# Kernel tuning notes

Measured on AMD Instinct MI355X. Metric: run time of the kernel, lower is better.

The kernel has to match this reference:

```python
import jax, jax.numpy as jnp
import numpy as np

N, E, IN, HID, OUT, H, R = 50000, 800000, 128, 64, 64, 4, 64
NEG_SLOPE = 0.2


def setup_inputs() -> dict:
    key = jax.random.key(0)
    ks = jax.random.split(key, 20)
    s = 0.05
    inp = {
        "x": jax.random.normal(ks[0], (N, IN), jnp.float32),
        "edge_index": jax.random.randint(ks[1], (2, E), 0, N, jnp.int32),
        "edge_type": jax.random.randint(ks[2], (E,), 0, R, jnp.int32),
        # layer 1 (in -> hidden)
        "rel1": jax.random.normal(ks[3], (R, IN), jnp.float32) * s,
        "W1": jax.random.normal(ks[4], (IN, H * HID), jnp.float32) * s,
        "We1": jax.random.normal(ks[5], (IN, H * HID), jnp.float32) * s,
        "as1": jax.random.normal(ks[6], (H, HID), jnp.float32) * s,
        "ad1": jax.random.normal(ks[7], (H, HID), jnp.float32) * s,
        "ae1": jax.random.normal(ks[8], (H, HID), jnp.float32) * s,
        "b1": jnp.zeros((HID,), jnp.float32),
        # layer 2 (hidden -> out)
        "rel2": jax.random.normal(ks[9], (R, HID), jnp.float32) * s,
        "W2": jax.random.normal(ks[10], (HID, H * OUT), jnp.float32) * s,
        "We2": jax.random.normal(ks[11], (HID, H * OUT), jnp.float32) * s,
        "as2": jax.random.normal(ks[12], (H, OUT), jnp.float32) * s,
        "ad2": jax.random.normal(ks[13], (H, OUT), jnp.float32) * s,
        "ae2": jax.random.normal(ks[14], (H, OUT), jnp.float32) * s,
        "b2": jnp.zeros((OUT,), jnp.float32),
    }
    return inp


def gat_layer(x, src, dst, edge_type, rel, W, We, a_s, a_d, a_e, b, C):
    # x: [N, Din] -> per-head features [N, H, C]
    xs = (x @ W).reshape(-1, H, C)
    alpha_src = jnp.einsum('nhc,hc->nh', xs, a_s)   # [N,H]
    alpha_dst = jnp.einsum('nhc,hc->nh', xs, a_d)   # [N,H]
    e = (rel[edge_type] @ We).reshape(-1, H, C)     # [E,H,C] projected edge feats
    alpha_e = jnp.einsum('ehc,hc->eh', e, a_e)      # [E,H]
    logits = alpha_src[src] + alpha_dst[dst] + alpha_e
    logits = jnp.where(logits >= 0, logits, NEG_SLOPE * logits)  # leaky_relu
    # segment softmax over destination nodes
    lmax = jax.ops.segment_max(logits, dst, num_segments=N)      # [N,H]
    ex = jnp.exp(logits - lmax[dst])
    den = jax.ops.segment_sum(ex, dst, num_segments=N)           # [N,H]
    w = ex / den[dst]                                            # [E,H]
    msg = w[:, :, None] * xs[src]                                # [E,H,C]
    out = jax.ops.segment_sum(msg, dst, num_segments=N)          # [N,H,C]
    return out.mean(axis=1) + b                                  # concat=False -> head mean


def reference(x, edge_index, edge_type, rel1, W1, We1, as1, ad1, ae1, b1,
              rel2, W2, We2, as2, ad2, ae2, b2):
    src, dst = edge_index[0], edge_index[1]
    h = gat_layer(x, src, dst, edge_type, rel1, W1, We1, as1, ad1, ae1, b1, HID)
    h = jax.nn.relu(h)
    out = gat_layer(h, src, dst, edge_type, rel2, W2, We2, as2, ad2, ae2, b2, OUT)
    return out
```

## Files before the change

kernel.cpp:

```cpp
#include <hip/hip_runtime.h>
#include <hip/hip_bf16.h>
#include <hip/hip_fp16.h>
#include <math.h>

#define N_NODES 50000
#define N_EDGES 800000
#define IN_DIM 128
#define NHEAD 4
#define NREL 64
#define HC 256
#define NEG_SLOPE 0.2f
#define SCAN_B ((N_NODES + 255) / 256)

using short8 = __attribute__((ext_vector_type(8))) short;
using f32x4  = __attribute__((ext_vector_type(4))) float;

__device__ __forceinline__ void load_lds16s(const short* g, short* l) {
  __builtin_amdgcn_global_load_lds(
      (const __attribute__((address_space(1))) unsigned int*)g,
      (__attribute__((address_space(3))) unsigned int*)l, 16, 0, 0);
}

__device__ __forceinline__ unsigned bf16rne(float v) {
  unsigned u = __float_as_uint(v);
  return (u + 0x7FFFu + ((u >> 16) & 1u)) >> 16;
}

__global__ __launch_bounds__(256) void prep_x(
    const float* __restrict__ X, short* __restrict__ Xh, short* __restrict__ Xl,
    int K) {
  __shared__ float plds[16 * 132];
  const int t = threadIdx.x;
  const int blk = blockIdx.x;
  const int LW = K + 4;
  for (int i = t * 4; i < 16 * K; i += 1024) {
    int r = i / K, k = i - r * K;
    *(float4*)&plds[r * LW + k] = *(const float4*)&X[(size_t)(blk * 16 + r) * K + k];
  }
  __syncthreads();
  for (int c = t; c < 2 * K; c += 256) {
    int p_k = c >> 6, l = c & 63;
    int r = l & 15, k0 = p_k * 32 + (l >> 4) * 8;
    unsigned hp[4], lp[4];
#pragma unroll
    for (int q = 0; q < 4; ++q) {
      float v0 = plds[r * LW + k0 + q * 2];
      float v1 = plds[r * LW + k0 + q * 2 + 1];
      unsigned h0 = bf16rne(v0), h1 = bf16rne(v1);
      float l0 = (v0 - __uint_as_float(h0 << 16)) * 256.0f;
      float l1 = (v1 - __uint_as_float(h1 << 16)) * 256.0f;
      hp[q] = h0 | (h1 << 16);
      lp[q] = bf16rne(l0) | (bf16rne(l1) << 16);
    }
    size_t base = ((size_t)(blk * (K >> 5) + p_k) * 64 + l) * 8;
    *(int4*)&Xh[base] = make_int4(hp[0], hp[1], hp[2], hp[3]);
    *(int4*)&Xl[base] = make_int4(lp[0], lp[1], lp[2], lp[3]);
  }
}

__global__ __launch_bounds__(256) void prep_w(
    const float* __restrict__ W, short* __restrict__ Wh, short* __restrict__ Wl,
    int K) {
  const int c = blockIdx.x * 256 + threadIdx.x;
  const int KP = K >> 5;
  if (c >= 16 * KP * 64) return;
  const int p = c >> 6, l = c & 63;
  const int p_c = p / KP, p_k = p - p_c * KP;
  const int col = p_c * 16 + (l & 15), k0 = p_k * 32 + (l >> 4) * 8;
  unsigned hp[4], lp[4];
#pragma unroll
  for (int q = 0; q < 4; ++q) {
    float v0 = W[(size_t)(k0 + q * 2) * HC + col];
    float v1 = W[(size_t)(k0 + q * 2 + 1) * HC + col];
    unsigned h0 = bf16rne(v0), h1 = bf16rne(v1);
    float l0 = (v0 - __uint_as_float(h0 << 16)) * 256.0f;
    float l1 = (v1 - __uint_as_float(h1 << 16)) * 256.0f;
    hp[q] = h0 | (h1 << 16);
    lp[q] = bf16rne(l0) | (bf16rne(l1) << 16);
  }
  size_t base = (size_t)c * 8;
  *(int4*)&Wh[base] = make_int4(hp[0], hp[1], hp[2], hp[3]);
  *(int4*)&Wl[base] = make_int4(lp[0], lp[1], lp[2], lp[3]);
}

__global__ __launch_bounds__(256, 4) void gemm_mfma(
    const short* __restrict__ Xh, const short* __restrict__ Xl,
    const short* __restrict__ Wh, const short* __restrict__ Wl,
    const float* __restrict__ a_s, const float* __restrict__ a_d,
    __half2* __restrict__ xs16, float* __restrict__ asrc, float* __restrict__ adst,
    int M, int K) {
  __shared__ short lds[2][24 * 512];
  const int t = threadIdx.x;
  const int wv = t >> 6, l = t & 63;
  const int KP = K >> 5;
  const int pr0 = blockIdx.x * 4;
  const int pc0 = blockIdx.y * 8;
  const int c0 = blockIdx.y * 128;

#define STAGE(BI, PK)                                                         \
  {                                                                           \
    _Pragma("unroll")                                                         \
    for (int j = 0; j < 6; ++j) {                                             \
      const int s = wv * 6 + j;                                               \
      const short* srcp;                                                      \
      if (s < 4)       srcp = Xh + (((size_t)(pr0 + s) * KP + (PK)) << 9);    \
      else if (s < 8)  srcp = Xl + (((size_t)(pr0 + s - 4) * KP + (PK)) << 9);\
      else if (s < 16) srcp = Wh + (((size_t)(pc0 + s - 8) * KP + (PK)) << 9);\
      else             srcp = Wl + (((size_t)(pc0 + s - 16) * KP + (PK)) << 9);\
      load_lds16s(srcp + l * 8, &lds[BI][s * 512]);                           \
    }                                                                         \
  }

  f32x4 acc0[8], acc1[8];
#pragma unroll
  for (int i = 0; i < 8; ++i)
#pragma unroll
    for (int c = 0; c < 4; ++c) { acc0[i][c] = 0.f; acc1[i][c] = 0.f; }

  STAGE(0, 0);
  for (int pk = 0; pk < KP; ++pk) {
    const int cur = pk & 1;
    if (pk + 1 < KP) {
      STAGE(cur ^ 1, pk + 1);
      asm volatile("s_waitcnt vmcnt(6)" ::: "memory");
    } else {
      asm volatile("s_waitcnt vmcnt(0)" ::: "memory");
    }
    __builtin_amdgcn_s_barrier();
    __builtin_amdgcn_sched_barrier(0);
    const short8 ah = *(const short8*)&lds[cur][(0 + wv) * 512 + l * 8];
    const short8 al = *(const short8*)&lds[cur][(4 + wv) * 512 + l * 8];
#pragma unroll
    for (int t8 = 0; t8 < 8; ++t8) {
      const short8 bh = *(const short8*)&lds[cur][(8 + t8) * 512 + l * 8];
      const short8 bl = *(const short8*)&lds[cur][(16 + t8) * 512 + l * 8];
      acc0[t8] = __builtin_amdgcn_mfma_f32_16x16x32_bf16(ah, bh, acc0[t8], 0, 0, 0);
      acc1[t8] = __builtin_amdgcn_mfma_f32_16x16x32_bf16(ah, bl, acc1[t8], 0, 0, 0);
      acc1[t8] = __builtin_amdgcn_mfma_f32_16x16x32_bf16(al, bh, acc1[t8], 0, 0, 0);
    }
    asm volatile("" ::: "memory");
    __builtin_amdgcn_s_barrier();
  }
#undef STAGE

  const int col_l = l & 15;
  const int row_l = (l >> 4) * 2 * 2;
  __half* xsh = (__half*)xs16;
  float asv[8], adv[8];
#pragma unroll
  for (int t8 = 0; t8 < 8; ++t8) {
    asv[t8] = a_s[c0 + t8 * 16 + col_l];
    adv[t8] = a_d[c0 + t8 * 16 + col_l];
  }
  float sp[2][4], dp[2][4];
#pragma unroll
  for (int hl = 0; hl < 2; ++hl)
#pragma unroll
    for (int r = 0; r < 4; ++r) { sp[hl][r] = 0.f; dp[hl][r] = 0.f; }

#pragma unroll
  for (int t8 = 0; t8 < 8; ++t8) {
    const int hl = t8 >> 2;
#pragma unroll
    for (int r = 0; r < 4; ++r) {
      const float v = acc0[t8][r] + acc1[t8][r] * (1.0f / 256.0f);
      const int row = (pr0 + wv) * 16 + row_l + r;
      if (row < M) {
        const int col = c0 + t8 * 16 + col_l;
        xsh[(size_t)row * HC + col] = __float2half(v);
      }
      sp[hl][r] += v * asv[t8];
      dp[hl][r] += v * adv[t8];
    }
  }
#pragma unroll
  for (int off = 1; off < 16; off <<= 1) {
#pragma unroll
    for (int hl = 0; hl < 2; ++hl)
#pragma unroll
      for (int r = 0; r < 4; ++r) {
        sp[hl][r] += __shfl_xor(sp[hl][r], off);
        dp[hl][r] += __shfl_xor(dp[hl][r], off);
      }
  }
  if (col_l == 0) {
#pragma unroll
    for (int hl = 0; hl < 2; ++hl) {
      const int head = blockIdx.y * 2 + hl;
#pragma unroll
      for (int r = 0; r < 4; ++r) {
        const int row = (pr0 + wv) * 16 + row_l + r;
        if (row < M) {
          asrc[row * NHEAD + head] = sp[hl][r];
          adst[row * NHEAD + head] = dp[hl][r];
        }
      }
    }
  }
}

__global__ __launch_bounds__(256) void relalpha2_kernel(
    const float* __restrict__ rel1, const float* __restrict__ We1, const float* __restrict__ ae1,
    const float* __restrict__ rel2, const float* __restrict__ We2, const float* __restrict__ ae2,
    float* __restrict__ tab1, float* __restrict__ tab2) {
  const int layer = blockIdx.x >> 6;
  const int r = blockIdx.x & 63;
  const float* rel = layer ? rel2 : rel1;
  const float* We  = layer ? We2  : We1;
  const float* ae  = layer ? ae2  : ae1;
  float* tab       = layer ? tab2 : tab1;
  const int K      = layer ? 64   : IN_DIM;
  int t = threadIdx.x;
  float acc = 0.f;
  for (int k = 0; k < K; ++k) acc += rel[(size_t)r * K + k] * We[(size_t)k * HC + t];
  int h = t >> 6, lane = t & 63;
  float p = acc * ae[t];
#pragma unroll
  for (int off = 32; off > 0; off >>= 1) p += __shfl_down(p, off);
  if (lane == 0) tab[r * NHEAD + h] = p;
}

__global__ __launch_bounds__(256) void hist_kernel(
    const int* __restrict__ dst, int* __restrict__ deg) {
  int e = blockIdx.x * blockDim.x + threadIdx.x;
  if (e < N_EDGES) atomicAdd(&deg[dst[e]], 1);
}

__global__ __launch_bounds__(256) void block_sum_kernel(
    const int* __restrict__ deg, int* __restrict__ bsum) {
  int i = blockIdx.x * 256 + threadIdx.x;
  int v = (i < N_NODES) ? deg[i] : 0;
#pragma unroll
  for (int off = 32; off > 0; off >>= 1) v += __shfl_down(v, off);
  __shared__ int w[4];
  if ((threadIdx.x & 63) == 0) w[threadIdx.x >> 6] = v;
  __syncthreads();
  if (threadIdx.x == 0) bsum[blockIdx.x] = w[0] + w[1] + w[2] + w[3];
}

__global__ __launch_bounds__(256) void scan_bsum_kernel(
    const int* __restrict__ bsum, int* __restrict__ boff) {
  __shared__ int s[256];
  int t = threadIdx.x;
  int v = (t < SCAN_B) ? bsum[t] : 0;
  s[t] = v;
  __syncthreads();
  for (int off = 1; off < 256; off <<= 1) {
    int u = (t >= off) ? s[t - off] : 0;
    __syncthreads();
    s[t] += u;
    __syncthreads();
  }
  boff[t] = (t == 0) ? 0 : s[t - 1];
}

__global__ __launch_bounds__(256) void scan_final_kernel(
    const int* __restrict__ deg, const int* __restrict__ boff,
    int* __restrict__ rowptr, int* __restrict__ cursor) {
  __shared__ int s[256];
  int t = threadIdx.x;
  int i = blockIdx.x * 256 + t;
  int v = (i < N_NODES) ? deg[i] : 0;
  s[t] = v;
  __syncthreads();
  for (int off = 1; off < 256; off <<= 1) {
    int u = (t >= off) ? s[t - off] : 0;
    __syncthreads();
    s[t] += u;
    __syncthreads();
  }
  int excl = boff[blockIdx.x] + s[t] - v;
  if (i < N_NODES) {
    rowptr[i] = excl;
    cursor[i] = excl;
  }
  if (t == 0 && blockIdx.x == 0) rowptr[N_NODES] = N_EDGES;
}

__global__ __launch_bounds__(256) void fill_kernel(
    const int* __restrict__ src, const int* __restrict__ dst,
    const int* __restrict__ etype, int* __restrict__ cursor,
    int2* __restrict__ csr_pack) {
  int e = blockIdx.x * blockDim.x + threadIdx.x;
  if (e >= N_EDGES) return;
  int d = dst[e];
  int i = atomicAdd(&cursor[d], 1);
  csr_pack[i] = make_int2(src[e], etype[e]);
}

__global__ __launch_bounds__(256) void gat_node_kernel(
    const int* __restrict__ rowptr, const int2* __restrict__ csr,
    const float* __restrict__ asrc, const float* __restrict__ adst,
    const float* __restrict__ tab, const __half2* __restrict__ xs16,
    const float* __restrict__ b, float* __restrict__ out, int relu) {
  const int n = (blockIdx.x * blockDim.x + threadIdx.x) >> 6;
  if (n >= N_NODES) return;
  const int lane = threadIdx.x & 63;
  const int hh = lane >> 4;
  const int cbase = lane << 2;
  const int i0 = rowptr[n], i1 = rowptr[n + 1];
  const float adn = adst[n * NHEAD + hh];
  const float treg = tab[lane * NHEAD + hh];

  float4 acc = make_float4(0.f, 0.f, 0.f, 0.f);
  float den = 0.f;
  int i = i0;
  for (; i + 4 <= i1; i += 4) {
    const int2 p0 = csr[i], p1 = csr[i + 1], p2 = csr[i + 2], p3 = csr[i + 3];
    float l0 = asrc[p0.x * NHEAD + hh] + adn + __shfl(treg, p0.y);
    float l1 = asrc[p1.x * NHEAD + hh] + adn + __shfl(treg, p1.y);
    float l2 = asrc[p2.x * NHEAD + hh] + adn + __shfl(treg, p2.y);
    float l3 = asrc[p3.x * NHEAD + hh] + adn + __shfl(treg, p3.y);
    const uint2 q0 = *(const uint2*)&xs16[((size_t)p0.x * HC + cbase) >> 1];
    const uint2 q1 = *(const uint2*)&xs16[((size_t)p1.x * HC + cbase) >> 1];
    const uint2 q2 = *(const uint2*)&xs16[((size_t)p2.x * HC + cbase) >> 1];
    const uint2 q3 = *(const uint2*)&xs16[((size_t)p3.x * HC + cbase) >> 1];
    l0 = (l0 >= 0.f) ? l0 : NEG_SLOPE * l0;
    l1 = (l1 >= 0.f) ? l1 : NEG_SLOPE * l1;
    l2 = (l2 >= 0.f) ? l2 : NEG_SLOPE * l2;
    l3 = (l3 >= 0.f) ? l3 : NEG_SLOPE * l3;
    const float w0 = __expf(l0), w1 = __expf(l1), w2 = __expf(l2), w3 = __expf(l3);
    den += (w0 + w1) + (w2 + w3);
    const float2 a0 = __half22float2(*(const __half2*)&q0.x), b0 = __half22float2(*(const __half2*)&q0.y);
    const float2 a1 = __half22float2(*(const __half2*)&q1.x), b1 = __half22float2(*(const __half2*)&q1.y);
    const float2 a2 = __half22float2(*(const __half2*)&q2.x), b2 = __half22float2(*(const __half2*)&q2.y);
    const float2 a3 = __half22float2(*(const __half2*)&q3.x), b3 = __half22float2(*(const __half2*)&q3.y);
    acc.x += w0 * a0.x + w1 * a1.x + w2 * a2.x + w3 * a3.x;
    acc.y += w0 * a0.y + w1 * a1.y + w2 * a2.y + w3 * a3.y;
    acc.z += w0 * b0.x + w1 * b1.x + w2 * b2.x + w3 * b3.x;
    acc.w += w0 * b0.y + w1 * b1.y + w2 * b2.y + w3 * b3.y;
  }
  for (; i < i1; ++i) {
    const int2 p = csr[i];
    float l = asrc[p.x * NHEAD + hh] + adn + __shfl(treg, p.y);
    l = (l >= 0.f) ? l : NEG_SLOPE * l;
    const float w = __expf(l);
    const uint2 q = *(const uint2*)&xs16[((size_t)p.x * HC + cbase) >> 1];
    const float2 a = __half22float2(*(const __half2*)&q.x);
    const float2 c = __half22float2(*(const __half2*)&q.y);
    den += w;
    acc.x += w * a.x; acc.y += w * a.y; acc.z += w * c.x; acc.w += w * c.y;
  }

  const float rd = (den > 0.f) ? (0.25f / den) : 0.f;
  float4 y = make_float4(acc.x * rd, acc.y * rd, acc.z * rd, acc.w * rd);
#pragma unroll
  for (int off = 16; off < 64; off <<= 1) {
    y.x += __shfl_xor(y.x, off);
    y.y += __shfl_xor(y.y, off);
    y.z += __shfl_xor(y.z, off);
    y.w += __shfl_xor(y.w, off);
  }
  if (lane < 16) {
    const float4 bb = *(const float4*)&b[lane * 4];
    y.x += bb.x; y.y += bb.y; y.z += bb.z; y.w += bb.w;
    if (relu) {
      y.x = fmaxf(y.x, 0.f); y.y = fmaxf(y.y, 0.f);
      y.z = fmaxf(y.z, 0.f); y.w = fmaxf(y.w, 0.f);
    }
    *(float4*)&out[(size_t)n * 64 + lane * 4] = y;
  }
}

extern "C" void kernel_launch(void* const* d_in, const int* in_sizes, int n_in,
                              void* d_out, int out_size, void* d_ws, size_t ws_size,
                              hipStream_t stream) {
  const float* x   = (const float*)d_in[0];
  const int* eidx  = (const int*)d_in[1];
  const int* etype = (const int*)d_in[2];
  const float* rel1 = (const float*)d_in[3];
  const float* W1   = (const float*)d_in[4];
  const float* We1  = (const float*)d_in[5];
  const float* as1  = (const float*)d_in[6];
  const float* ad1  = (const float*)d_in[7];
  const float* ae1  = (const float*)d_in[8];
  const float* b1   = (const float*)d_in[9];
  const float* rel2 = (const float*)d_in[10];
  const float* W2   = (const float*)d_in[11];
  const float* We2  = (const float*)d_in[12];
  const float* as2  = (const float*)d_in[13];
  const float* ad2  = (const float*)d_in[14];
  const float* ae2  = (const float*)d_in[15];
  const float* b2   = (const float*)d_in[16];
  const int* src = eidx;
  const int* dst = eidx + N_EDGES;

  char* wsb = (char*)d_ws;
  size_t off = 0;
  auto carve = [&](size_t bytes) { char* p = wsb + off; off = (off + bytes + 255) & ~(size_t)255; return p; };
  __half2* xs16 = (__half2*)carve((size_t)N_NODES * HC * 2);
  float* asrc = (float*)carve((size_t)N_NODES * NHEAD * 4);
  float* adst = (float*)carve((size_t)N_NODES * NHEAD * 4);
  float* tab1 = (float*)carve(NREL * NHEAD * 4);
  float* tab2 = (float*)carve(NREL * NHEAD * 4);
  float* h1   = (float*)carve((size_t)N_NODES * 64 * 4);
  short* xfh  = (short*)carve(((size_t)N_NODES * IN_DIM + 32768) * 2);
  short* xfl  = (short*)carve(((size_t)N_NODES * IN_DIM + 32768) * 2);
  short* w1h  = (short*)carve(256 * IN_DIM * 2);
  short* w1l  = (short*)carve(256 * IN_DIM * 2);
  short* w2h  = (short*)carve(256 * 64 * 2);
  short* w2l  = (short*)carve(256 * 64 * 2);
  int* deg    = (int*)carve(N_NODES * 4);
  int* rowptr = (int*)carve((N_NODES + 1) * 4);
  int* cursor = (int*)carve(N_NODES * 4);
  int2* csr   = (int2*)carve((size_t)N_EDGES * 8);
  int* bsum   = (int*)carve(256 * 4);
  int* boff   = (int*)carve(256 * 4);

  hipMemsetAsync(deg, 0, N_NODES * sizeof(int), stream);
  hist_kernel<<<(N_EDGES + 255) / 256, 256, 0, stream>>>(dst, deg);
  block_sum_kernel<<<SCAN_B, 256, 0, stream>>>(deg, bsum);
  scan_bsum_kernel<<<1, 256, 0, stream>>>(bsum, boff);
  scan_final_kernel<<<SCAN_B, 256, 0, stream>>>(deg, boff, rowptr, cursor);
  fill_kernel<<<(N_EDGES + 255) / 256, 256, 0, stream>>>(src, dst, etype, cursor, csr);
  relalpha2_kernel<<<2 * NREL, 256, 0, stream>>>(rel1, We1, ae1, rel2, We2, ae2, tab1, tab2);
  prep_w<<<(16 * (IN_DIM >> 5) * 64 + 255) / 256, 256, 0, stream>>>(W1, w1h, w1l, IN_DIM);
  prep_w<<<(16 * (64 >> 5) * 64 + 255) / 256, 256, 0, stream>>>(W2, w2h, w2l, 64);

  const dim3 gemm_grid((N_NODES + 63) / 64, 2);
  const int GB = (N_NODES * 64 + 255) / 256;
  const int XB = N_NODES / 16;

  prep_x<<<XB, 256, 0, stream>>>(x, xfh, xfl, IN_DIM);
  gemm_mfma<<<gemm_grid, 256, 0, stream>>>(xfh, xfl, w1h, w1l, as1, ad1, xs16, asrc, adst, N_NODES, IN_DIM);
  gat_node_kernel<<<GB, 256, 0, stream>>>(rowptr, csr, asrc, adst, tab1, xs16, b1, h1, 1);

  prep_x<<<XB, 256, 0, stream>>>(h1, xfh, xfl, 64);
  gemm_mfma<<<gemm_grid, 256, 0, stream>>>(xfh, xfl, w2h, w2l, as2, ad2, xs16, asrc, adst, N_NODES, 64);
  gat_node_kernel<<<GB, 256, 0, stream>>>(rowptr, csr, asrc, adst, tab2, xs16, b2, (float*)d_out, 0);
}
```

Baseline: 318.6 us.

## Fuse prep kernels, merge CSR fill into GEMM, emit bf16 split from layer-1

Several small setup kernels (x split, degree histogram, relation alpha table, W splits) are merged into one launch with block-range dispatch. The CSR fill runs as extra blocks in the first GEMM launch, and layer-1 aggregation writes the hi/lo bf16 tiled layout directly, so the h1 buffer and the second prep_x pass go away. This cuts launch count and a full read/write of the hidden activations. In exchange, heterogeneous blocks share one launch, and the fill's atomics now run alongside MFMA work.

New measurement: 309.5 us. 2.9% less time.

```diff
diff --git a/kernel.cpp b/kernel.cpp
--- a/kernel.cpp
+++ b/kernel.cpp
@@ -11,6 +11,9 @@
 #define HC 256
 #define NEG_SLOPE 0.2f
 #define SCAN_B ((N_NODES + 255) / 256)
+#define XB (N_NODES / 16)
+#define HB ((N_EDGES + 255) / 256)
+#define GEMM_BLKS (((N_NODES + 63) / 64) * 2)
 
 using short8 = __attribute__((ext_vector_type(8))) short;
 using f32x4  = __attribute__((ext_vector_type(4))) float;
@@ -26,76 +29,120 @@
   return (u + 0x7FFFu + ((u >> 16) & 1u)) >> 16;
 }
 
-__global__ __launch_bounds__(256) void prep_x(
-    const float* __restrict__ X, short* __restrict__ Xh, short* __restrict__ Xl,
-    int K) {
+__global__ __launch_bounds__(256) void fused_prep(
+    const float* __restrict__ x, short* __restrict__ xfh, short* __restrict__ xfl,
+    const int* __restrict__ dst, int* __restrict__ deg,
+    const float* __restrict__ rel1, const float* __restrict__ We1, const float* __restrict__ ae1,
+    const float* __restrict__ rel2, const float* __restrict__ We2, const float* __restrict__ ae2,
+    float* __restrict__ tab1, float* __restrict__ tab2,
+    const float* __restrict__ W1, short* __restrict__ w1h, short* __restrict__ w1l,
+    const float* __restrict__ W2, short* __restrict__ w2h, short* __restrict__ w2l) {
+  const int bid = blockIdx.x;
+  const int t = threadIdx.x;
   __shared__ float plds[16 * 132];
-  const int t = threadIdx.x;
-  const int blk = blockIdx.x;
-  const int LW = K + 4;
-  for (int i = t * 4; i < 16 * K; i += 1024) {
-    int r = i / K, k = i - r * K;
-    *(float4*)&plds[r * LW + k] = *(const float4*)&X[(size_t)(blk * 16 + r) * K + k];
-  }
-  __syncthreads();
-  for (int c = t; c < 2 * K; c += 256) {
-    int p_k = c >> 6, l = c & 63;
-    int r = l & 15, k0 = p_k * 32 + (l >> 4) * 8;
+
+  if (bid < XB) {
+    const int K = IN_DIM, LW = K + 4;
+    for (int i = t * 4; i < 16 * K; i += 1024) {
+      int r = i / K, k = i - r * K;
+      *(float4*)&plds[r * LW + k] = *(const float4*)&x[(size_t)(bid * 16 + r) * K + k];
+    }
+    __syncthreads();
+    for (int c = t; c < 2 * K; c += 256) {
+      int p_k = c >> 6, l = c & 63;
+      int r = l & 15, k0 = p_k * 32 + (l >> 4) * 8;
+      unsigned hp[4], lp[4];
+#pragma unroll
+      for (int q = 0; q < 4; ++q) {
+        float v0 = plds[r * LW + k0 + q * 2];
+        float v1 = plds[r * LW + k0 + q * 2 + 1];
+        unsigned h0 = bf16rne(v0), h1 = bf16rne(v1);
+        float l0 = (v0 - __uint_as_float(h0 << 16)) * 256.0f;
+        float l1 = (v1 - __uint_as_float(h1 << 16)) * 256.0f;
+        hp[q] = h0 | (h1 << 16);
+        lp[q] = bf16rne(l0) | (bf16rne(l1) << 16);
+      }
+      size_t base = ((size_t)(bid * (K >> 5) + p_k) * 64 + l) * 8;
+      *(int4*)&xfh[base] = make_int4(hp[0], hp[1], hp[2], hp[3]);
+      *(int4*)&xfl[base] = make_int4(lp[0], lp[1], lp[2], lp[3]);
+    }
+    return;
+  }
+  if (bid < XB + HB) {
+    const int e = (bid - XB) * 256 + t;
+    if (e < N_EDGES) atomicAdd(&deg[dst[e]], 1);
+    return;
+  }
+  if (bid < XB + HB + 128) {
+    const int rb = bid - (XB + HB);
+    const int layer = rb >> 6, r = rb & 63;
+    const float* rel = layer ? rel2 : rel1;
+    const float* We  = layer ? We2  : We1;
+    const float* ae  = layer ? ae2  : ae1;
+    float* tab       = layer ? tab2 : tab1;
+    const int K      = layer ? 64   : IN_DIM;
+    float acc = 0.f;
+    for (int k = 0; k < K; ++k) acc += rel[(size_t)r * K + k] * We[(size_t)k * HC + t];
+    int h = t >> 6, lane = t & 63;
+    float p = acc * ae[t];
+#pragma unroll
+    for (int off = 32; off > 0; off >>= 1) p += __shfl_down(p, off);
+    if (lane == 0) tab[r * NHEAD + h] = p;
+    return;
+  }
+  {
+    const int wb = bid - (XB + HB + 128);
+    const float* W; short* Wh; short* Wl; int K, c;
+    if (wb < 16) { W = W1; Wh = w1h; Wl = w1l; K = IN_DIM; c = wb * 256 + t; }
+    else         { W = W2; Wh = w2h; Wl = w2l; K = 64;     c = (wb - 16) * 256 + t; }
+    const int KP = K >> 5;
+    if (c >= 16 * KP * 64) return;
+    const int p = c >> 6, l = c & 63;
+    const int p_c = p / KP, p_k = p - p_c * KP;
+    const int col = p_c * 16 + (l & 15), k0 = p_k * 32 + (l >> 4) * 8;
     unsigned hp[4], lp[4];
 #pragma unroll
     for (int q = 0; q < 4; ++q) {
-      float v0 = plds[r * LW + k0 + q * 2];
-      float v1 = plds[r * LW + k0 + q * 2 + 1];
+      float v0 = W[(size_t)(k0 + q * 2) * HC + col];
+      float v1 = W[(size_t)(k0 + q * 2 + 1) * HC + col];
       unsigned h0 = bf16rne(v0), h1 = bf16rne(v1);
       float l0 = (v0 - __uint_as_float(h0 << 16)) * 256.0f;
       float l1 = (v1 - __uint_as_float(h1 << 16)) * 256.0f;
       hp[q] = h0 | (h1 << 16);
       lp[q] = bf16rne(l0) | (bf16rne(l1) << 16);
     }
-    size_t base = ((size_t)(blk * (K >> 5) + p_k) * 64 + l) * 8;
-    *(int4*)&Xh[base] = make_int4(hp[0], hp[1], hp[2], hp[3]);
-    *(int4*)&Xl[base] = make_int4(lp[0], lp[1], lp[2], lp[3]);
-  }
-}
-
-__global__ __launch_bounds__(256) void prep_w(
-    const float* __restrict__ W, short* __restrict__ Wh, short* __restrict__ Wl,
-    int K) {
-  const int c = blockIdx.x * 256 + threadIdx.x;
-  const int KP = K >> 5;
-  if (c >= 16 * KP * 64) return;
-  const int p = c >> 6, l = c & 63;
-  const int p_c = p / KP, p_k = p - p_c * KP;
-  const int col = p_c * 16 + (l & 15), k0 = p_k * 32 + (l >> 4) * 8;
-  unsigned hp[4], lp[4];
-#pragma unroll
-  for (int q = 0; q < 4; ++q) {
-    float v0 = W[(size_t)(k0 + q * 2) * HC + col];
-    float v1 = W[(size_t)(k0 + q * 2 + 1) * HC + col];
-    unsigned h0 = bf16rne(v0), h1 = bf16rne(v1);
-    float l0 = (v0 - __uint_as_float(h0 << 16)) * 256.0f;
-    float l1 = (v1 - __uint_as_float(h1 << 16)) * 256.0f;
-    hp[q] = h0 | (h1 << 16);
-    lp[q] = bf16rne(l0) | (bf16rne(l1) << 16);
-  }
-  size_t base = (size_t)c * 8;
-  *(int4*)&Wh[base] = make_int4(hp[0], hp[1], hp[2], hp[3]);
-  *(int4*)&Wl[base] = make_int4(lp[0], lp[1], lp[2], lp[3]);
-}
-
-__global__ __launch_bounds__(256, 4) void gemm_mfma(
+    size_t base = (size_t)c * 8;
+    *(int4*)&Wh[base] = make_int4(hp[0], hp[1], hp[2], hp[3]);
+    *(int4*)&Wl[base] = make_int4(lp[0], lp[1], lp[2], lp[3]);
+  }
+}
+
+__global__ __launch_bounds__(256, 4) void gemm_fill(
     const short* __restrict__ Xh, const short* __restrict__ Xl,
     const short* __restrict__ Wh, const short* __restrict__ Wl,
     const float* __restrict__ a_s, const float* __restrict__ a_d,
     __half2* __restrict__ xs16, float* __restrict__ asrc, float* __restrict__ adst,
-    int M, int K) {
+    int M, int K,
+    const int* __restrict__ src, const int* __restrict__ dstv,
+    const int* __restrict__ etype, int* __restrict__ cursor,
+    int2* __restrict__ csr) {
   __shared__ short lds[2][24 * 512];
+  const int bid = blockIdx.x;
   const int t = threadIdx.x;
+  if (bid >= GEMM_BLKS) {
+    const int e = (bid - GEMM_BLKS) * 256 + t;
+    if (e < N_EDGES) {
+      const int d = dstv[e];
+      const int i = atomicAdd(&cursor[d], 1);
+      csr[i] = make_int2(src[e], etype[e]);
+    }
+    return;
+  }
   const int wv = t >> 6, l = t & 63;
   const int KP = K >> 5;
-  const int pr0 = blockIdx.x * 4;
-  const int pc0 = blockIdx.y * 8;
-  const int c0 = blockIdx.y * 128;
+  const int pr0 = (bid >> 1) * 4;
+  const int pc0 = (bid & 1) * 8;
+  const int c0 = (bid & 1) * 128;
 
 #define STAGE(BI, PK)                                                         \
   {                                                                           \
@@ -144,7 +191,7 @@
 #undef STAGE
 
   const int col_l = l & 15;
-  const int row_l = (l >> 4) * 2 * 2;
+  const int row_l = (l >> 4) * 4;
   __half* xsh = (__half*)xs16;
   float asv[8], adv[8];
 #pragma unroll
@@ -186,7 +233,7 @@
   if (col_l == 0) {
 #pragma unroll
     for (int hl = 0; hl < 2; ++hl) {
-      const int head = blockIdx.y * 2 + hl;
+      const int head = (bid & 1) * 2 + hl;
 #pragma unroll
       for (int r = 0; r < 4; ++r) {
         const int row = (pr0 + wv) * 16 + row_l + r;
@@ -197,33 +244,6 @@
       }
     }
   }
-}
-
-__global__ __launch_bounds__(256) void relalpha2_kernel(
-    const float* __restrict__ rel1, const float* __restrict__ We1, const float* __restrict__ ae1,
-    const float* __restrict__ rel2, const float* __restrict__ We2, const float* __restrict__ ae2,
-    float* __restrict__ tab1, float* __restrict__ tab2) {
-  const int layer = blockIdx.x >> 6;
-  const int r = blockIdx.x & 63;
-  const float* rel = layer ? rel2 : rel1;
-  const float* We  = layer ? We2  : We1;
-  const float* ae  = layer ? ae2  : ae1;
-  float* tab       = layer ? tab2 : tab1;
-  const int K      = layer ? 64   : IN_DIM;
-  int t = threadIdx.x;
-  float acc = 0.f;
-  for (int k = 0; k < K; ++k) acc += rel[(size_t)r * K + k] * We[(size_t)k * HC + t];
-  int h = t >> 6, lane = t & 63;
-  float p = acc * ae[t];
-#pragma unroll
-  for (int off = 32; off > 0; off >>= 1) p += __shfl_down(p, off);
-  if (lane == 0) tab[r * NHEAD + h] = p;
-}
-
-__global__ __launch_bounds__(256) void hist_kernel(
-    const int* __restrict__ dst, int* __restrict__ deg) {
-  int e = blockIdx.x * blockDim.x + threadIdx.x;
-  if (e < N_EDGES) atomicAdd(&deg[dst[e]], 1);
 }
 
 __global__ __launch_bounds__(256) void block_sum_kernel(
@@ -277,22 +297,12 @@
   if (t == 0 && blockIdx.x == 0) rowptr[N_NODES] = N_EDGES;
 }
 
-__global__ __launch_bounds__(256) void fill_kernel(
-    const int* __restrict__ src, const int* __restrict__ dst,
-    const int* __restrict__ etype, int* __restrict__ cursor,
-    int2* __restrict__ csr_pack) {
-  int e = blockIdx.x * blockDim.x + threadIdx.x;
-  if (e >= N_EDGES) return;
-  int d = dst[e];
-  int i = atomicAdd(&cursor[d], 1);
-  csr_pack[i] = make_int2(src[e], etype[e]);
-}
-
 __global__ __launch_bounds__(256) void gat_node_kernel(
     const int* __restrict__ rowptr, const int2* __restrict__ csr,
     const float* __restrict__ asrc, const float* __restrict__ adst,
     const float* __restrict__ tab, const __half2* __restrict__ xs16,
-    const float* __restrict__ b, float* __restrict__ out, int relu) {
+    const float* __restrict__ b, float* __restrict__ out,
+    short* __restrict__ oxh, short* __restrict__ oxl, int mode) {
   const int n = (blockIdx.x * blockDim.x + threadIdx.x) >> 6;
   if (n >= N_NODES) return;
   const int lane = threadIdx.x & 63;
@@ -354,11 +364,27 @@
   if (lane < 16) {
     const float4 bb = *(const float4*)&b[lane * 4];
     y.x += bb.x; y.y += bb.y; y.z += bb.z; y.w += bb.w;
-    if (relu) {
+    if (mode) {
       y.x = fmaxf(y.x, 0.f); y.y = fmaxf(y.y, 0.f);
       y.z = fmaxf(y.z, 0.f); y.w = fmaxf(y.w, 0.f);
-    }
-    *(float4*)&out[(size_t)n * 64 + lane * 4] = y;
+      unsigned h0 = bf16rne(y.x), h1 = bf16rne(y.y);
+      unsigned h2 = bf16rne(y.z), h3 = bf16rne(y.w);
+      float l0 = (y.x - __uint_as_float(h0 << 16)) * 256.0f;
+      float l1 = (y.y - __uint_as_float(h1 << 16)) * 256.0f;
+      float l2 = (y.z - __uint_as_float(h2 << 16)) * 256.0f;
+      float l3 = (y.w - __uint_as_float(h3 << 16)) * 256.0f;
+      unsigned hp0 = h0 | (h1 << 16), hp1 = h2 | (h3 << 16);
+      unsigned lp0 = bf16rne(l0) | (bf16rne(l1) << 16);
+      unsigned lp1 = bf16rne(l2) | (bf16rne(l3) << 16);
+      const int pk = lane >> 3;
+      const int lip = (n & 15) + ((lane >> 1) & 3) * 16;
+      const int j0 = (lane & 1) * 4;
+      size_t base = ((size_t)((n >> 4) * 2 + pk) * 64 + lip) * 8 + j0;
+      *(uint2*)&oxh[base] = make_uint2(hp0, hp1);
+      *(uint2*)&oxl[base] = make_uint2(lp0, lp1);
+    } else {
+      *(float4*)&out[(size_t)n * 64 + lane * 4] = y;
+    }
   }
 }
 
@@ -393,7 +419,6 @@
   float* adst = (float*)carve((size_t)N_NODES * NHEAD * 4);
   float* tab1 = (float*)carve(NREL * NHEAD * 4);
   float* tab2 = (float*)carve(NREL * NHEAD * 4);
-  float* h1   = (float*)carve((size_t)N_NODES * 64 * 4);
   short* xfh  = (short*)carve(((size_t)N_NODES * IN_DIM + 32768) * 2);
   short* xfl  = (short*)carve(((size_t)N_NODES * IN_DIM + 32768) * 2);
   short* w1h  = (short*)carve(256 * IN_DIM * 2);
@@ -408,24 +433,27 @@
   int* boff   = (int*)carve(256 * 4);
 
   hipMemsetAsync(deg, 0, N_NODES * sizeof(int), stream);
-  hist_kernel<<<(N_EDGES + 255) / 256, 256, 0, stream>>>(dst, deg);
+
+  fused_prep<<<XB + HB + 128 + 16 + 8, 256, 0, stream>>>(
+      x, xfh, xfl, dst, deg,
+      rel1, We1, ae1, rel2, We2, ae2, tab1, tab2,
+      W1, w1h, w1l, W2, w2h, w2l);
+
   block_sum_kernel<<<SCAN_B, 256, 0, stream>>>(deg, bsum);
   scan_bsum_kernel<<<1, 256, 0, stream>>>(bsum, boff);
   scan_final_kernel<<<SCAN_B, 256, 0, stream>>>(deg, boff, rowptr, cursor);
-  fill_kernel<<<(N_EDGES + 255) / 256, 256, 0, stream>>>(src, dst, etype, cursor, csr);
-  relalpha2_kernel<<<2 * NREL, 256, 0, stream>>>(rel1, We1, ae1, rel2, We2, ae2, tab1, tab2);
-  prep_w<<<(16 * (IN_DIM >> 5) * 64 + 255) / 256, 256, 0, stream>>>(W1, w1h, w1l, IN_DIM);
-  prep_w<<<(16 * (64 >> 5) * 64 + 255) / 256, 256, 0, stream>>>(W2, w2h, w2l, 64);
-
-  const dim3 gemm_grid((N_NODES + 63) / 64, 2);
+
   const int GB = (N_NODES * 64 + 255) / 256;
-  const int XB = N_NODES / 16;
-
-  prep_x<<<XB, 256, 0, stream>>>(x, xfh, xfl, IN_DIM);
-  gemm_mfma<<<gemm_grid, 256, 0, stream>>>(xfh, xfl, w1h, w1l, as1, ad1, xs16, asrc, adst, N_NODES, IN_DIM);
-  gat_node_kernel<<<GB, 256, 0, stream>>>(rowptr, csr, asrc, adst, tab1, xs16, b1, h1, 1);
-
-  prep_x<<<XB, 256, 0, stream>>>(h1, xfh, xfl, 64);
-  gemm_mfma<<<gemm_grid, 256, 0, stream>>>(xfh, xfl, w2h, w2l, as2, ad2, xs16, asrc, adst, N_NODES, 64);
-  gat_node_kernel<<<GB, 256, 0, stream>>>(rowptr, csr, asrc, adst, tab2, xs16, b2, (float*)d_out, 0);
-}
+
+  gemm_fill<<<GEMM_BLKS + HB, 256, 0, stream>>>(
+      xfh, xfl, w1h, w1l, as1, ad1, xs16, asrc, adst, N_NODES, IN_DIM,
+      src, dst, etype, cursor, csr);
+  gat_node_kernel<<<GB, 256, 0, stream>>>(rowptr, csr, asrc, adst, tab1, xs16,
+                                          b1, nullptr, xfh, xfl, 1);
+
+  gemm_fill<<<GEMM_BLKS, 256, 0, stream>>>(
+      xfh, xfl, w2h, w2l, as2, ad2, xs16, asrc, adst, N_NODES, 64,
+      src, dst, etype, cursor, csr);
+  gat_node_kernel<<<GB, 256, 0, stream>>>(rowptr, csr, asrc, adst, tab2, xs16,
+                                          b2, (float*)d_out, nullptr, nullptr, 0);
+}
```
